# Performance work log

Measured on AMD Instinct MI355X. Metric: run time of the kernel, lower is better.

## Reference

```python
import jax, jax.numpy as jnp
import numpy as np

N_GRAPHS = 256
N_NODES = 100000
N_EDGES = 1000000
EMB = 64
EMB_RBF = 16
NUM_HEADS = 1


def setup_inputs() -> dict:
    key = jax.random.key(0)
    ks = jax.random.split(key, 10)
    edge_emb = jax.random.normal(ks[0], (N_EDGES, EMB), dtype=jnp.float32)
    edge_index = jax.random.randint(ks[1], (2, N_EDGES), 0, N_NODES, dtype=jnp.int64)
    distance_vec = jax.random.normal(ks[2], (N_EDGES, 3), dtype=jnp.float32)
    lattice = jax.random.normal(ks[3], (N_GRAPHS, 3, 3), dtype=jnp.float32)
    batch = jnp.sort(jax.random.randint(ks[4], (N_NODES,), 0, N_GRAPHS, dtype=jnp.int64))
    rbf = jax.random.uniform(ks[5], (N_EDGES, EMB_RBF), dtype=jnp.float32)
    # Dense layers (GemNet Dense defaults to bias=False)
    s = 1.0 / np.sqrt(EMB)
    W1 = jax.random.normal(ks[6], (EMB, EMB), dtype=jnp.float32) * s
    W2 = jax.random.normal(ks[7], (EMB, EMB), dtype=jnp.float32) * s
    W_rbf = jax.random.normal(ks[8], (EMB_RBF, EMB), dtype=jnp.float32) * (1.0 / np.sqrt(EMB_RBF))
    W_out = jax.random.normal(ks[9], (EMB, NUM_HEADS), dtype=jnp.float32) * s
    return {"edge_emb": edge_emb, "edge_index": edge_index, "distance_vec": distance_vec,
            "lattice": lattice, "batch": batch, "rbf": rbf,
            "W1": W1, "W2": W2, "W_rbf": W_rbf, "W_out": W_out}


def reference(edge_emb, edge_index, distance_vec, lattice, batch, rbf, W1, W2, W_rbf, W_out):
    # compute_score_per_edge: MLP on edge embeddings, gated by RBF projection
    h = jax.nn.silu(edge_emb @ W1)            # [E, EMB]
    x_F = h @ W2                               # [E, EMB]
    x_F = x_F * (rbf @ W_rbf)                  # RBF gate, [E, EMB]
    edge_scores = x_F @ W_out                  # [E, num_heads]

    batch_edge = batch[edge_index[0]]          # graph id per edge, [E]
    # normalize_score=True: divide by edge count per graph
    num_edges = jax.ops.segment_sum(jnp.ones((edge_scores.shape[0],), dtype=edge_scores.dtype),
                                    batch_edge, num_segments=N_GRAPHS)
    edge_scores = edge_scores / num_edges[batch_edge, None]

    # edge_score_to_lattice_score_frac_symmetric, summed over heads (num_heads=1)
    s = edge_scores[:, 0]                      # [E]
    unit = distance_vec / jnp.linalg.norm(distance_vec, axis=-1, keepdims=True)
    outer = s[:, None, None] * unit[:, :, None] * distance_vec[:, None, :]  # [E,3,3]
    sym = 0.5 * (outer + jnp.swapaxes(outer, 1, 2))
    out = jax.ops.segment_sum(sym, batch_edge, num_segments=N_GRAPHS)       # [B,3,3]
    return out
```

## Files before the change

### kernel.cpp

```cpp
#include <hip/hip_runtime.h>
#include <math.h>

constexpr int G    = 256;
constexpr int EMB  = 64;
constexpr int ERBF = 16;

typedef __attribute__((ext_vector_type(8))) short bf16x8;
typedef __attribute__((ext_vector_type(4))) float f32x4;

static __device__ __forceinline__ short bf16_rne(float f) {
    union { float f; unsigned u; } v; v.f = f;
    unsigned r = (v.u + 0x7FFFu + ((v.u >> 16) & 1u)) >> 16;
    return (short)r;
}

__global__ void prep_M_kernel(const float* __restrict__ W2,
                              const float* __restrict__ W_rbf,
                              const float* __restrict__ W_out,
                              float* __restrict__ M) {
    int t = blockIdx.x * blockDim.x + threadIdx.x;
    if (t >= EMB * ERBF) return;
    int p = t >> 4;
    int k = t & 15;
    float acc = 0.f;
    for (int j = 0; j < EMB; ++j)
        acc = fmaf(W2[p * EMB + j] * W_out[j], W_rbf[k * EMB + j], acc);
    M[p * ERBF + k] = acc;
}

__global__ __launch_bounds__(256, 4) void edge_kernel(
    const float* __restrict__ edge_emb,
    const int*   __restrict__ edge_src,
    const float* __restrict__ dvec,
    const int*   __restrict__ batch,
    const float* __restrict__ rbf,
    const float* __restrict__ W1,
    const float* __restrict__ M,
    float* __restrict__ partial,
    int ne, int nblk)
{
    constexpr int HSTRIDE = 72;
    __shared__ short hT[4][16 * HSTRIDE];
    __shared__ float accs[G * 9];

    const int tid  = threadIdx.x;
    const int w    = tid >> 6;
    const int lane = tid & 63;
    const int q    = lane >> 4;
    const int col  = lane & 15;

    for (int i = tid; i < G * 9; i += 256) accs[i] = 0.f;

    bf16x8 w1f[4][2];
#pragma unroll
    for (int nt = 0; nt < 4; ++nt)
#pragma unroll
        for (int c = 0; c < 2; ++c) {
            bf16x8 wv;
#pragma unroll
            for (int j = 0; j < 8; ++j)
                wv[j] = bf16_rne(W1[(c * 32 + q * 8 + j) * EMB + nt * 16 + col]);
            w1f[nt][c] = wv;
        }
    bf16x8 mf[2];
#pragma unroll
    for (int c = 0; c < 2; ++c) {
        bf16x8 mv;
#pragma unroll
        for (int j = 0; j < 8; ++j)
            mv[j] = bf16_rne(M[(c * 32 + q * 8 + j) * ERBF + col]);
        mf[c] = mv;
    }
    __syncthreads();

    const long tiles_step = (long)nblk * 64;
    for (long tbase = (long)blockIdx.x * 64; tbase < ne; tbase += tiles_step) {
        const long e0 = tbase + (long)w * 16;

        bf16x8 af[2];
        const long erow = e0 + col;
        const bool rowok = (erow < ne);
#pragma unroll
        for (int c = 0; c < 2; ++c) {
            bf16x8 a;
            if (rowok) {
                const float4* p = (const float4*)(edge_emb + (size_t)erow * EMB + c * 32 + q * 8);
                float4 v0 = p[0], v1 = p[1];
                a[0] = bf16_rne(v0.x); a[1] = bf16_rne(v0.y);
                a[2] = bf16_rne(v0.z); a[3] = bf16_rne(v0.w);
                a[4] = bf16_rne(v1.x); a[5] = bf16_rne(v1.y);
                a[6] = bf16_rne(v1.z); a[7] = bf16_rne(v1.w);
            } else {
#pragma unroll
                for (int j = 0; j < 8; ++j) a[j] = 0;
            }
            af[c] = a;
        }

        f32x4 hacc[4];
#pragma unroll
        for (int nt = 0; nt < 4; ++nt) {
            f32x4 z = {0.f, 0.f, 0.f, 0.f};
            z = __builtin_amdgcn_mfma_f32_16x16x32_bf16(af[0], w1f[nt][0], z, 0, 0, 0);
            z = __builtin_amdgcn_mfma_f32_16x16x32_bf16(af[1], w1f[nt][1], z, 0, 0, 0);
            hacc[nt] = z;
        }

#pragma unroll
        for (int nt = 0; nt < 4; ++nt)
#pragma unroll
            for (int r = 0; r < 4; ++r) {
                float x = hacc[nt][r];
                float s = x * __builtin_amdgcn_rcpf(1.f + __expf(-x));
                hT[w][(q * 4 + r) * HSTRIDE + nt * 16 + col] = bf16_rne(s);
            }
        __syncthreads();

        f32x4 tacc = {0.f, 0.f, 0.f, 0.f};
#pragma unroll
        for (int c = 0; c < 2; ++c) {
            const bf16x8* ap = (const bf16x8*)&hT[w][col * HSTRIDE + c * 32 + q * 8];
            tacc = __builtin_amdgcn_mfma_f32_16x16x32_bf16(*ap, mf[c], tacc, 0, 0, 0);
        }

        float sc[4];
#pragma unroll
        for (int r = 0; r < 4; ++r) {
            long e = e0 + q * 4 + r;
            float rv = (e < ne) ? rbf[(size_t)e * ERBF + col] : 0.f;
            sc[r] = tacc[r] * rv;
        }
#pragma unroll
        for (int m = 1; m < 16; m <<= 1) {
#pragma unroll
            for (int r = 0; r < 4; ++r) sc[r] += __shfl_xor(sc[r], m);
        }

        if (col < 4) {
            long e = e0 + q * 4 + col;
            if (e < ne) {
                float s = sc[col];
                int   g = batch[edge_src[e]];
                size_t de = (size_t)e * 3;
                float dx = dvec[de], dy = dvec[de + 1], dz = dvec[de + 2];
                float nrm = sqrtf(dx * dx + dy * dy + dz * dz);
                float cc = s / nrm;
                float* a = &accs[g * 9];
                atomicAdd(a + 0, cc * dx * dx);
                atomicAdd(a + 1, cc * dx * dy);
                atomicAdd(a + 2, cc * dx * dz);
                atomicAdd(a + 3, cc * dy * dy);
                atomicAdd(a + 4, cc * dy * dz);
                atomicAdd(a + 5, cc * dz * dz);
                atomicAdd(a + 6, 1.0f);
            }
        }
        __syncthreads();
    }

    float* outp = partial + (size_t)blockIdx.x * (G * 8);
    {
        int g = tid;
        float* a = &accs[g * 9];
        float4 p0 = {a[0], a[1], a[2], a[3]};
        float4 p1 = {a[4], a[5], a[6], 0.f};
        ((float4*)(outp + g * 8))[0] = p0;
        ((float4*)(outp + g * 8))[1] = p1;
    }
}

__global__ __launch_bounds__(256) void reduce_kernel(
    const float* __restrict__ partial, float* __restrict__ out, int nblk)
{
    int g = blockIdx.x;
    __shared__ float red[256][8];
    float loc[8];
#pragma unroll
    for (int c = 0; c < 8; ++c) loc[c] = 0.f;

    for (int b = threadIdx.x; b < nblk; b += 256) {
        const float4* p = (const float4*)(partial + (size_t)b * (G * 8) + g * 8);
        float4 v0 = p[0], v1 = p[1];
        loc[0] += v0.x; loc[1] += v0.y; loc[2] += v0.z; loc[3] += v0.w;
        loc[4] += v1.x; loc[5] += v1.y; loc[6] += v1.z; loc[7] += v1.w;
    }
#pragma unroll
    for (int c = 0; c < 8; ++c) red[threadIdx.x][c] = loc[c];
    __syncthreads();

    for (int off = 128; off >= 1; off >>= 1) {
        if (threadIdx.x < off) {
#pragma unroll
            for (int c = 0; c < 8; ++c)
                red[threadIdx.x][c] += red[threadIdx.x + off][c];
        }
        __syncthreads();
    }

    if (threadIdx.x == 0) {
        float cnt = red[0][6];
        float inv = (cnt > 0.f) ? (1.f / cnt) : 0.f;
        float xx = red[0][0] * inv, xy = red[0][1] * inv, xz = red[0][2] * inv;
        float yy = red[0][3] * inv, yz = red[0][4] * inv, zz = red[0][5] * inv;
        float* o = out + g * 9;
        o[0] = xx; o[1] = xy; o[2] = xz;
        o[3] = xy; o[4] = yy; o[5] = yz;
        o[6] = xz; o[7] = yz; o[8] = zz;
    }
}

extern "C" void kernel_launch(void* const* d_in, const int* in_sizes, int n_in,
                              void* d_out, int out_size, void* d_ws, size_t ws_size,
                              hipStream_t stream) {
    const float* edge_emb   = (const float*)d_in[0];
    const int*   edge_index = (const int*)  d_in[1];
    const float* dvec       = (const float*)d_in[2];
    const int*   batch      = (const int*)  d_in[4];
    const float* rbf        = (const float*)d_in[5];
    const float* W1         = (const float*)d_in[6];
    const float* W2         = (const float*)d_in[7];
    const float* W_rbf      = (const float*)d_in[8];
    const float* W_out      = (const float*)d_in[9];
    float* out = (float*)d_out;

    int ne = in_sizes[0] / EMB;

    float* M = (float*)d_ws;
    float* partial = (float*)((char*)d_ws + 4096);
    size_t avail = (ws_size > 4096) ? (ws_size - 4096) : 0;
    int nblk = (int)(avail / (G * 8 * sizeof(float)));
    int tiles = (ne + 63) / 64;
    if (nblk > 1024)  nblk = 1024;
    if (nblk > tiles) nblk = tiles;
    if (nblk < 1)     nblk = 1;

    prep_M_kernel<<<4, 256, 0, stream>>>(W2, W_rbf, W_out, M);
    edge_kernel<<<nblk, 256, 0, stream>>>(edge_emb, edge_index, dvec, batch,
                                          rbf, W1, M, partial, ne, nblk);
    reduce_kernel<<<G, 256, 0, stream>>>(partial, out, nblk);
}
```

Baseline: 428.5 us.

## Compute RBF gate by MFMA and drop LDS transpose and per-tile barriers

Instead of staging SiLU(h) in LDS and multiplying by M, each wave projects rbf through M^T with one MFMA per output tile, producing a per-column gate in registers. It then dots it with SiLU(h) directly in the accumulator layout. This removes the shared-memory round trip and both per-iteration __syncthreads, letting waves advance independently over edge tiles. The rbf input is now rounded to bf16 before the gate product, and LDS atomics into accs may race more freely across waves, which was already safe.

```diff
diff --git a/kernel.cpp b/kernel.cpp
--- a/kernel.cpp
+++ b/kernel.cpp
@@ -39,8 +39,6 @@
     float* __restrict__ partial,
     int ne, int nblk)
 {
-    constexpr int HSTRIDE = 72;
-    __shared__ short hT[4][16 * HSTRIDE];
     __shared__ float accs[G * 9];
 
     const int tid  = threadIdx.x;
@@ -62,24 +60,25 @@
                 wv[j] = bf16_rne(W1[(c * 32 + q * 8 + j) * EMB + nt * 16 + col]);
             w1f[nt][c] = wv;
         }
-    bf16x8 mf[2];
-#pragma unroll
-    for (int c = 0; c < 2; ++c) {
+    bf16x8 mtf[4];
+#pragma unroll
+    for (int nt = 0; nt < 4; ++nt) {
         bf16x8 mv;
 #pragma unroll
-        for (int j = 0; j < 8; ++j)
-            mv[j] = bf16_rne(M[(c * 32 + q * 8 + j) * ERBF + col]);
-        mf[c] = mv;
+        for (int j = 0; j < 8; ++j) {
+            int k = q * 8 + j;
+            mv[j] = (k < ERBF) ? bf16_rne(M[(nt * 16 + col) * ERBF + k]) : (short)0;
+        }
+        mtf[nt] = mv;
     }
     __syncthreads();
 
-    const long tiles_step = (long)nblk * 64;
-    for (long tbase = (long)blockIdx.x * 64; tbase < ne; tbase += tiles_step) {
-        const long e0 = tbase + (long)w * 16;
+    const long estep = (long)nblk * 4 * 16;
+    for (long e0 = ((long)blockIdx.x * 4 + w) * 16; e0 < ne; e0 += estep) {
+        const long erow  = e0 + col;
+        const bool rowok = (erow < ne);
 
         bf16x8 af[2];
-        const long erow = e0 + col;
-        const bool rowok = (erow < ne);
 #pragma unroll
         for (int c = 0; c < 2; ++c) {
             bf16x8 a;
@@ -96,39 +95,41 @@
             }
             af[c] = a;
         }
-
-        f32x4 hacc[4];
+        bf16x8 rf;
+        if (q < 2 && rowok) {
+            const float4* p = (const float4*)(rbf + (size_t)erow * ERBF + q * 8);
+            float4 v0 = p[0], v1 = p[1];
+            rf[0] = bf16_rne(v0.x); rf[1] = bf16_rne(v0.y);
+            rf[2] = bf16_rne(v0.z); rf[3] = bf16_rne(v0.w);
+            rf[4] = bf16_rne(v1.x); rf[5] = bf16_rne(v1.y);
+            rf[6] = bf16_rne(v1.z); rf[7] = bf16_rne(v1.w);
+        } else {
+#pragma unroll
+            for (int j = 0; j < 8; ++j) rf[j] = 0;
+        }
+
+        f32x4 hacc[4], vacc[4];
 #pragma unroll
         for (int nt = 0; nt < 4; ++nt) {
             f32x4 z = {0.f, 0.f, 0.f, 0.f};
             z = __builtin_amdgcn_mfma_f32_16x16x32_bf16(af[0], w1f[nt][0], z, 0, 0, 0);
             z = __builtin_amdgcn_mfma_f32_16x16x32_bf16(af[1], w1f[nt][1], z, 0, 0, 0);
             hacc[nt] = z;
-        }
-
-#pragma unroll
-        for (int nt = 0; nt < 4; ++nt)
-#pragma unroll
-            for (int r = 0; r < 4; ++r) {
+            f32x4 zv = {0.f, 0.f, 0.f, 0.f};
+            vacc[nt] = __builtin_amdgcn_mfma_f32_16x16x32_bf16(rf, mtf[nt], zv, 0, 0, 0);
+        }
+
+        float sc[4];
+#pragma unroll
+        for (int r = 0; r < 4; ++r) {
+            float acc = 0.f;
+#pragma unroll
+            for (int nt = 0; nt < 4; ++nt) {
                 float x = hacc[nt][r];
                 float s = x * __builtin_amdgcn_rcpf(1.f + __expf(-x));
-                hT[w][(q * 4 + r) * HSTRIDE + nt * 16 + col] = bf16_rne(s);
+                acc = fmaf(s, vacc[nt][r], acc);
             }
-        __syncthreads();
-
-        f32x4 tacc = {0.f, 0.f, 0.f, 0.f};
-#pragma unroll
-        for (int c = 0; c < 2; ++c) {
-            const bf16x8* ap = (const bf16x8*)&hT[w][col * HSTRIDE + c * 32 + q * 8];
-            tacc = __builtin_amdgcn_mfma_f32_16x16x32_bf16(*ap, mf[c], tacc, 0, 0, 0);
-        }
-
-        float sc[4];
-#pragma unroll
-        for (int r = 0; r < 4; ++r) {
-            long e = e0 + q * 4 + r;
-            float rv = (e < ne) ? rbf[(size_t)e * ERBF + col] : 0.f;
-            sc[r] = tacc[r] * rv;
+            sc[r] = acc;
         }
 #pragma unroll
         for (int m = 1; m < 16; m <<= 1) {
@@ -155,9 +156,9 @@
                 atomicAdd(a + 6, 1.0f);
             }
         }
-        __syncthreads();
-    }
-
+    }
+
+    __syncthreads();
     float* outp = partial + (size_t)blockIdx.x * (G * 8);
     {
         int g = tid;
```

Measured after the change: 426.8 us. Within noise of the previous version (-0.4%).
